# Kernel optimization log

Hardware: AMD Instinct MI355X
Metric: run time of the kernel (lower is better)

## Reference

```python
import jax, jax.numpy as jnp
import numpy as np

D_MODEL = 1024
NUM_HEADS = 16
HEAD_DIM = D_MODEL // NUM_HEADS  # used only for score scaling, as in the torch code


def setup_inputs() -> dict:
    key = jax.random.key(0)
    ks = jax.random.split(key, 8)
    B, S, D = 4, 2048, D_MODEL
    w_scale = 1.0 / np.sqrt(D)
    return {
        "x": jax.random.normal(ks[0], (B, S, D), dtype=jnp.float32),
        "Wq": jax.random.normal(ks[1], (D, D), dtype=jnp.float32) * w_scale,
        "bq": jnp.zeros((D,), dtype=jnp.float32),
        "Wk": jax.random.normal(ks[2], (D, D), dtype=jnp.float32) * w_scale,
        "bk": jnp.zeros((D,), dtype=jnp.float32),
        "Wv": jax.random.normal(ks[3], (D, D), dtype=jnp.float32) * w_scale,
        "bv": jnp.zeros((D,), dtype=jnp.float32),
        "temperature_scale": jnp.ones((1,), dtype=jnp.float32),
    }


def reference(x, Wq, bq, Wk, bk, Wv, bv, temperature_scale):
    # q, k, v: (B, S, D) -- no head split in the original module
    q = x @ Wq + bq
    k = x @ Wk + bk
    v = x @ Wv + bv
    scale = jnp.asarray(HEAD_DIM, x.dtype) ** 0.5
    # scores: (B, S, S)
    scores = jnp.einsum("bqd,bkd->bqk", q, k) / scale / temperature_scale[0]
    probs = jax.nn.softmax(scores, axis=-1)
    # per-row attention entropy (B, S, 1)
    entropy = -jnp.sum(probs * jnp.log(probs + 1e-8), axis=-1, keepdims=True)
    attention_output = jnp.einsum("bqk,bkd->bqd", probs, v)
    return attention_output, entropy.mean()
```

## Files before the change

kernel.cpp:

```cpp
#include <hip/hip_runtime.h>
#include <hip/hip_bf16.h>
#include <cstdint>
#include <cstddef>


typedef __attribute__((ext_vector_type(8))) short short8;
typedef __attribute__((ext_vector_type(4))) short short4v;
typedef __attribute__((ext_vector_type(4))) float f32x4;

#define GLOBAL_AS __attribute__((address_space(1)))
#define LDS_AS __attribute__((address_space(3)))

__device__ __forceinline__ void async_load16(const void* g, void* lds) {
  __builtin_amdgcn_global_load_lds((GLOBAL_AS void*)g, (LDS_AS void*)lds, 16, 0, 0);
}

__device__ __forceinline__ short f2bf_s(float x) {
  __hip_bfloat16 h = __float2bfloat16(x);
  return *reinterpret_cast<short*>(&h);
}

template <int MODE>
__device__ __forceinline__
void gemm_body(const __hip_bfloat16* __restrict__ A,
               const __hip_bfloat16* __restrict__ Bt,
               void* __restrict__ Cout,
               const float* __restrict__ bias,
               int K, int lda, int ldb, int ldc,
               __hip_bfloat16* __restrict__ sA,
               __hip_bfloat16* __restrict__ sB,
               int m0, int n0,
               const float* __restrict__ aux,
               float* __restrict__ stats) {
  const int tid  = threadIdx.x;
  const int lane = tid & 63;
  const int wid  = tid >> 6;
  const int wm = (wid >> 1) * 64;
  const int wn = (wid & 1) * 64;
  const int quad = lane >> 4;
  const int rc   = lane & 15;

  f32x4 acc[4][4] = {};

  const int srow = tid >> 2;
  const int scol = ((tid & 3) ^ ((tid >> 3) & 3)) * 8;
  const __hip_bfloat16* Ag0 = A  + (size_t)(m0 + srow) * lda + scol;
  const __hip_bfloat16* Ag1 = Ag0 + (size_t)64 * lda;
  const __hip_bfloat16* Bg0 = Bt + (size_t)(n0 + srow) * ldb + scol;
  const __hip_bfloat16* Bg1 = Bg0 + (size_t)64 * ldb;
  __hip_bfloat16* sA0 = &sA[wid * 512];
  __hip_bfloat16* sA1 = &sA[2048 + wid * 512];
  __hip_bfloat16* sB0 = &sB[wid * 512];
  __hip_bfloat16* sB1 = &sB[2048 + wid * 512];

  const int q_sw = (quad ^ ((rc >> 1) & 3)) * 8;

  for (int k0 = 0; k0 < K; k0 += 32) {
    async_load16(Ag0 + k0, sA0);
    async_load16(Ag1 + k0, sA1);
    async_load16(Bg0 + k0, sB0);
    async_load16(Bg1 + k0, sB1);
    __syncthreads();

    short8 af[4], bf[4];
#pragma unroll
    for (int i = 0; i < 4; ++i)
      af[i] = *(const short8*)&sA[(wm + i * 16 + rc) * 32 + q_sw];
#pragma unroll
    for (int i = 0; i < 4; ++i)
      bf[i] = *(const short8*)&sB[(wn + i * 16 + rc) * 32 + q_sw];

#pragma unroll
    for (int mi = 0; mi < 4; ++mi)
#pragma unroll
      for (int ni = 0; ni < 4; ++ni)
        acc[mi][ni] = __builtin_amdgcn_mfma_f32_16x16x32_bf16(
            af[mi], bf[ni], acc[mi][ni], 0, 0, 0);
    __syncthreads();
  }

  if (MODE == 3) {
    const float inv_scale = 1.0f / (8.0f * aux[0]);
    float l_acc[4][4] = {}, w_acc[4][4] = {};
#pragma unroll
    for (int mi = 0; mi < 4; ++mi)
#pragma unroll
      for (int ni = 0; ni < 4; ++ni)
#pragma unroll
        for (int r = 0; r < 4; ++r) {
          const float xv = acc[mi][ni][r] * inv_scale;
          const float e = __expf(xv);
          acc[mi][ni][r] = e;
          l_acc[mi][r] += e;
          w_acc[mi][r] += e * xv;
        }
    const int chunk = (n0 + wn) >> 6;
#pragma unroll
    for (int mi = 0; mi < 4; ++mi)
#pragma unroll
      for (int r = 0; r < 4; ++r) {
        float l = l_acc[mi][r], w = w_acc[mi][r];
#pragma unroll
        for (int off = 1; off < 16; off <<= 1) {
          l += __shfl_xor(l, off);
          w += __shfl_xor(w, off);
        }
        if (rc == 0) {
          const int row = m0 + wm + mi * 16 + quad * 4 + r;
          *(float2*)&stats[((size_t)row * 32 + chunk) * 2] = make_float2(l, w);
        }
      }
#pragma unroll
    for (int mi = 0; mi < 4; ++mi)
#pragma unroll
      for (int ni = 0; ni < 4; ++ni) {
        const int col = n0 + wn + ni * 16 + rc;
#pragma unroll
        for (int r = 0; r < 4; ++r) {
          const int row = m0 + wm + mi * 16 + quad * 4 + r;
          ((__hip_bfloat16*)Cout)[(size_t)row * ldc + col] =
              __float2bfloat16(acc[mi][ni][r]);
        }
      }
  } else if (MODE == 4) {
#pragma unroll
    for (int mi = 0; mi < 4; ++mi) {
      float sc[4];
#pragma unroll
      for (int r = 0; r < 4; ++r)
        sc[r] = aux[m0 + wm + mi * 16 + quad * 4 + r];
#pragma unroll
      for (int ni = 0; ni < 4; ++ni) {
        const int col = n0 + wn + ni * 16 + rc;
#pragma unroll
        for (int r = 0; r < 4; ++r) {
          const int row = m0 + wm + mi * 16 + quad * 4 + r;
          ((float*)Cout)[(size_t)row * ldc + col] = acc[mi][ni][r] * sc[r];
        }
      }
    }
  } else {
#pragma unroll
    for (int mi = 0; mi < 4; ++mi) {
#pragma unroll
      for (int ni = 0; ni < 4; ++ni) {
        const int col = n0 + wn + ni * 16 + rc;
        const float badd = bias[col];
        if (MODE == 2) {
          const int rowb = m0 + wm + mi * 16 + quad * 4;
          short4v o;
#pragma unroll
          for (int r = 0; r < 4; ++r) o[r] = f2bf_s(acc[mi][ni][r] + badd);
          const size_t idx = (size_t)(rowb >> 11) * (1024u * 2048u) +
                             (size_t)col * 2048u + (size_t)(rowb & 2047);
          *(short4v*)((short*)Cout + idx) = o;
        } else {
#pragma unroll
          for (int r = 0; r < 4; ++r) {
            const int row = m0 + wm + mi * 16 + quad * 4 + r;
            ((__hip_bfloat16*)Cout)[(size_t)row * ldc + col] =
                __float2bfloat16(acc[mi][ni][r] + badd);
          }
        }
      }
    }
  }
}


__global__ __launch_bounds__(256)
void qkv_fused(const __hip_bfloat16* __restrict__ xb,
               const __hip_bfloat16* __restrict__ Wt,
               __hip_bfloat16* __restrict__ qb, __hip_bfloat16* __restrict__ kb,
               __hip_bfloat16* __restrict__ vt,
               const float* __restrict__ bq, const float* __restrict__ bk,
               const float* __restrict__ bv) {
  __shared__ __align__(16) __hip_bfloat16 sA[128 * 32];
  __shared__ __align__(16) __hip_bfloat16 sB[128 * 32];
  const int lin = blockIdx.x;
  const int j = lin & 7, t = lin >> 3;
  const int x = t & 7;
  const int G = j + 8 * (t >> 3);
  const int z = G >> 6, y = G & 63;
  const int m0 = y * 128, n0 = x * 128;

  const __hip_bfloat16* B = Wt + (size_t)z * 1024 * 1024;
  if (z == 0)
    gemm_body<1>(xb, B, qb, bq, 1024, 1024, 1024, 1024, sA, sB, m0, n0, nullptr, nullptr);
  else if (z == 1)
    gemm_body<1>(xb, B, kb, bk, 1024, 1024, 1024, 1024, sA, sB, m0, n0, nullptr, nullptr);
  else
    gemm_body<2>(xb, B, vt, bv, 1024, 1024, 1024, 0, sA, sB, m0, n0, nullptr, nullptr);
}

__global__ __launch_bounds__(256)
void scores_swz(const __hip_bfloat16* __restrict__ qb,
                const __hip_bfloat16* __restrict__ kb,
                __hip_bfloat16* __restrict__ Pt,
                const float* __restrict__ tptr,
                float* __restrict__ stats) {
  __shared__ __align__(16) __hip_bfloat16 sA[128 * 32];
  __shared__ __align__(16) __hip_bfloat16 sB[128 * 32];
  const int lin = blockIdx.x;
  const int j = lin & 7, t = lin >> 3;
  const int w = t & 15;
  const int G = j + 8 * (t >> 4);
  const size_t z = G >> 4;
  const int r = G & 15;
  const int y = (r >> 2) * 4 + (w >> 2);
  const int x = (r & 3) * 4 + (w & 3);
  gemm_body<3>(qb + z * 2048 * 1024, kb + z * 2048 * 1024,
               Pt + z * 2048 * 2048, nullptr, 1024, 1024, 1024, 2048,
               sA, sB, y * 128, x * 128, tptr, stats + z * 2048 * 64);
}

__global__ __launch_bounds__(256)
void pv_swz(const __hip_bfloat16* __restrict__ Pt,
            const __hip_bfloat16* __restrict__ vt,
            float* __restrict__ out,
            const float* __restrict__ inv_l) {
  __shared__ __align__(16) __hip_bfloat16 sA[128 * 32];
  __shared__ __align__(16) __hip_bfloat16 sB[128 * 32];
  const int lin = blockIdx.x;
  const int j = lin & 7, t = lin >> 3;
  const int w = t & 3;
  const int G = j + 8 * (t >> 2);
  const size_t z = G >> 5;
  const int r = G & 31;
  const int y = (r >> 2) * 2 + (w >> 1);
  const int x = (r & 3) * 2 + (w & 1);
  gemm_body<4>(Pt + z * 2048 * 2048, vt + z * 1024 * 2048,
               out + z * 2048 * 1024, nullptr, 2048, 2048, 2048, 1024,
               sA, sB, y * 128, x * 128, inv_l + z * 2048, nullptr);
}

__global__ __launch_bounds__(256)
void cast_f32_to_bf16(const float* __restrict__ src,
                      __hip_bfloat16* __restrict__ dst, int n) {
  const int i = (blockIdx.x * 256 + threadIdx.x) * 8;
  if (i >= n) return;
  const float4 a = *(const float4*)(src + i);
  const float4 b = *(const float4*)(src + i + 4);
  short8 o;
  o[0] = f2bf_s(a.x); o[1] = f2bf_s(a.y); o[2] = f2bf_s(a.z); o[3] = f2bf_s(a.w);
  o[4] = f2bf_s(b.x); o[5] = f2bf_s(b.y); o[6] = f2bf_s(b.z); o[7] = f2bf_s(b.w);
  *(short8*)((short*)dst + i) = o;
}

__global__ __launch_bounds__(256)
void transpose_cast_3w(const float* __restrict__ Wq, const float* __restrict__ Wk,
                       const float* __restrict__ Wv,
                       __hip_bfloat16* __restrict__ Wt) {
  __shared__ float tile[64][65];
  const int z = blockIdx.z;
  const float* src = (z == 0) ? Wq : (z == 1) ? Wk : Wv;
  __hip_bfloat16* dst = Wt + (size_t)z * 1024 * 1024;
  const int c0 = blockIdx.x * 64;
  const int r0 = blockIdx.y * 64;
  const int lane = threadIdx.x & 63;
  const int grp  = threadIdx.x >> 6;
#pragma unroll
  for (int i = 0; i < 16; ++i) {
    const int r = grp * 16 + i;
    tile[r][lane] = src[(size_t)(r0 + r) * 1024 + c0 + lane];
  }
  __syncthreads();
#pragma unroll
  for (int i = 0; i < 16; ++i) {
    const int r = grp * 16 + i;
    dst[(size_t)(c0 + r) * 1024 + r0 + lane] = __float2bfloat16(tile[lane][r]);
  }
}

__global__ __launch_bounds__(256)
void stats_reduce(const float* __restrict__ stats,
                  float* __restrict__ inv_l, float* __restrict__ Hrow) {
  const int row = blockIdx.x * 256 + threadIdx.x;
  const float* sp = stats + (size_t)row * 64;
  float l = 0.f, w = 0.f;
#pragma unroll
  for (int j = 0; j < 16; ++j) {
    const float4 a = *(const float4*)(sp + j * 4);
    l += a.x + a.z;
    w += a.y + a.w;
  }
  const float il = 1.0f / l;
  inv_l[row] = il;
  Hrow[row] = __logf(l) - w * il;
}

__global__ __launch_bounds__(256)
void reduce_entropy(const float* __restrict__ Hrow, float* __restrict__ out) {
  const int tid  = threadIdx.x;
  const int lane = tid & 63;
  const int wid  = tid >> 6;
  float s = 0.f;
#pragma unroll
  for (int j = 0; j < 8; ++j) {
    const float4 a = *(const float4*)(Hrow + j * 1024 + tid * 4);
    s += a.x + a.y + a.z + a.w;
  }
#pragma unroll
  for (int off = 1; off < 64; off <<= 1) s += __shfl_xor(s, off);
  __shared__ float red[4];
  if (lane == 0) red[wid] = s;
  __syncthreads();
  if (tid == 0)
    out[0] = (red[0] + red[1] + red[2] + red[3]) * (1.0f / 8192.0f);
}

extern "C" void kernel_launch(void* const* d_in, const int* in_sizes, int n_in,
                              void* d_out, int out_size, void* d_ws, size_t ws_size,
                              hipStream_t stream) {
  const float* x    = (const float*)d_in[0];
  const float* Wq   = (const float*)d_in[1];
  const float* bq   = (const float*)d_in[2];
  const float* Wk   = (const float*)d_in[3];
  const float* bk   = (const float*)d_in[4];
  const float* Wv   = (const float*)d_in[5];
  const float* bv   = (const float*)d_in[6];
  const float* temp = (const float*)d_in[7];
  float* out = (float*)d_out;
  char* ws = (char*)d_ws;

  __hip_bfloat16* qb    = (__hip_bfloat16*)(ws + 0);
  __hip_bfloat16* kb    = (__hip_bfloat16*)(ws + 16777216);
  __hip_bfloat16* vt    = (__hip_bfloat16*)(ws + 33554432);
  __hip_bfloat16* xb    = (__hip_bfloat16*)(ws + 50331648);
  __hip_bfloat16* Wt    = (__hip_bfloat16*)(ws + 67108864);
  __hip_bfloat16* Pt    = (__hip_bfloat16*)(ws + 73400320);
  float*          stats = (float*)(ws + 106954752);
  float*          inv_l = (float*)(ws + 109051904);
  float*          Hrow  = (float*)(ws + 109084672);

  cast_f32_to_bf16<<<4096, 256, 0, stream>>>(x, xb, 8388608);
  transpose_cast_3w<<<dim3(16, 16, 3), 256, 0, stream>>>(Wq, Wk, Wv, Wt);

  qkv_fused<<<1536, 256, 0, stream>>>(xb, Wt, qb, kb, vt, bq, bk, bv);

  scores_swz<<<1024, 256, 0, stream>>>(qb, kb, Pt, temp, stats);
  stats_reduce<<<32, 256, 0, stream>>>(stats, inv_l, Hrow);
  pv_swz<<<512, 256, 0, stream>>>(Pt, vt, out, inv_l);

  reduce_entropy<<<1, 256, 0, stream>>>(Hrow, out + 8388608);
}
```

Baseline: 274.6 us.

## Double K-tile depth to 64 and fold score scaling into Q projection

The shared GEMM body now stages a 64-wide K slice per iteration with an 8-way XOR swizzle, halving the number of barrier pairs per tile and issuing two MFMA rounds per sync. The 1/(sqrt(d)*temperature) score scale is applied once when Q is written instead of on every score element, and the scores epilogue is restructured per row-block to reduce live registers. LDS use doubles to 32 KB per block, which may lower occupancy, and rounding Q after scaling changes bf16 rounding slightly.

```diff
diff --git a/kernel.cpp b/kernel.cpp
--- a/kernel.cpp
+++ b/kernel.cpp
@@ -42,64 +42,58 @@
 
   f32x4 acc[4][4] = {};
 
-  const int srow = tid >> 2;
-  const int scol = ((tid & 3) ^ ((tid >> 3) & 3)) * 8;
-  const __hip_bfloat16* Ag0 = A  + (size_t)(m0 + srow) * lda + scol;
-  const __hip_bfloat16* Ag1 = Ag0 + (size_t)64 * lda;
-  const __hip_bfloat16* Bg0 = Bt + (size_t)(n0 + srow) * ldb + scol;
-  const __hip_bfloat16* Bg1 = Bg0 + (size_t)64 * ldb;
-  __hip_bfloat16* sA0 = &sA[wid * 512];
-  __hip_bfloat16* sA1 = &sA[2048 + wid * 512];
-  __hip_bfloat16* sB0 = &sB[wid * 512];
-  __hip_bfloat16* sB1 = &sB[2048 + wid * 512];
-
-  const int q_sw = (quad ^ ((rc >> 1) & 3)) * 8;
-
-  for (int k0 = 0; k0 < K; k0 += 32) {
-    async_load16(Ag0 + k0, sA0);
-    async_load16(Ag1 + k0, sA1);
-    async_load16(Bg0 + k0, sB0);
-    async_load16(Bg1 + k0, sB1);
+  const int srow = tid >> 3;
+  const int scol = ((tid & 7) ^ ((tid >> 3) & 7)) * 8;
+  const __hip_bfloat16* Ag = A  + (size_t)(m0 + srow) * lda + scol;
+  const __hip_bfloat16* Bg = Bt + (size_t)(n0 + srow) * ldb + scol;
+
+  for (int k0 = 0; k0 < K; k0 += 64) {
+#pragma unroll
+    for (int p = 0; p < 4; ++p) {
+      async_load16(Ag + k0 + (size_t)(32 * p) * lda, &sA[(wid * 64 + 256 * p) * 8]);
+      async_load16(Bg + k0 + (size_t)(32 * p) * ldb, &sB[(wid * 64 + 256 * p) * 8]);
+    }
     __syncthreads();
 
-    short8 af[4], bf[4];
-#pragma unroll
-    for (int i = 0; i < 4; ++i)
-      af[i] = *(const short8*)&sA[(wm + i * 16 + rc) * 32 + q_sw];
-#pragma unroll
-    for (int i = 0; i < 4; ++i)
-      bf[i] = *(const short8*)&sB[(wn + i * 16 + rc) * 32 + q_sw];
-
-#pragma unroll
-    for (int mi = 0; mi < 4; ++mi)
+#pragma unroll
+    for (int kk = 0; kk < 2; ++kk) {
+      const int xo = ((kk * 4 + quad) ^ (rc & 7)) * 8;
+      short8 af[4], bf[4];
+#pragma unroll
+      for (int i = 0; i < 4; ++i)
+        af[i] = *(const short8*)&sA[(wm + i * 16 + rc) * 64 + xo];
+#pragma unroll
+      for (int i = 0; i < 4; ++i)
+        bf[i] = *(const short8*)&sB[(wn + i * 16 + rc) * 64 + xo];
+
+#pragma unroll
+      for (int mi = 0; mi < 4; ++mi)
+#pragma unroll
+        for (int ni = 0; ni < 4; ++ni)
+          acc[mi][ni] = __builtin_amdgcn_mfma_f32_16x16x32_bf16(
+              af[mi], bf[ni], acc[mi][ni], 0, 0, 0);
+    }
+    __syncthreads();
+  }
+
+  if (MODE == 3) {
+    const int chunk = (n0 + wn) >> 6;
+#pragma unroll
+    for (int mi = 0; mi < 4; ++mi) {
+      float l_acc[4] = {}, w_acc[4] = {};
 #pragma unroll
       for (int ni = 0; ni < 4; ++ni)
-        acc[mi][ni] = __builtin_amdgcn_mfma_f32_16x16x32_bf16(
-            af[mi], bf[ni], acc[mi][ni], 0, 0, 0);
-    __syncthreads();
-  }
-
-  if (MODE == 3) {
-    const float inv_scale = 1.0f / (8.0f * aux[0]);
-    float l_acc[4][4] = {}, w_acc[4][4] = {};
-#pragma unroll
-    for (int mi = 0; mi < 4; ++mi)
-#pragma unroll
-      for (int ni = 0; ni < 4; ++ni)
 #pragma unroll
         for (int r = 0; r < 4; ++r) {
-          const float xv = acc[mi][ni][r] * inv_scale;
+          const float xv = acc[mi][ni][r];
           const float e = __expf(xv);
           acc[mi][ni][r] = e;
-          l_acc[mi][r] += e;
-          w_acc[mi][r] += e * xv;
-        }
-    const int chunk = (n0 + wn) >> 6;
-#pragma unroll
-    for (int mi = 0; mi < 4; ++mi)
+          l_acc[r] += e;
+          w_acc[r] += e * xv;
+        }
 #pragma unroll
       for (int r = 0; r < 4; ++r) {
-        float l = l_acc[mi][r], w = w_acc[mi][r];
+        float l = l_acc[r], w = w_acc[r];
 #pragma unroll
         for (int off = 1; off < 16; off <<= 1) {
           l += __shfl_xor(l, off);
@@ -110,8 +104,6 @@
           *(float2*)&stats[((size_t)row * 32 + chunk) * 2] = make_float2(l, w);
         }
       }
-#pragma unroll
-    for (int mi = 0; mi < 4; ++mi)
 #pragma unroll
       for (int ni = 0; ni < 4; ++ni) {
         const int col = n0 + wn + ni * 16 + rc;
@@ -122,6 +114,7 @@
               __float2bfloat16(acc[mi][ni][r]);
         }
       }
+    }
   } else if (MODE == 4) {
 #pragma unroll
     for (int mi = 0; mi < 4; ++mi) {
@@ -140,6 +133,7 @@
       }
     }
   } else {
+    const float qsc = (MODE == 1 && aux) ? 1.0f / (8.0f * aux[0]) : 1.0f;
 #pragma unroll
     for (int mi = 0; mi < 4; ++mi) {
 #pragma unroll
@@ -159,7 +153,7 @@
           for (int r = 0; r < 4; ++r) {
             const int row = m0 + wm + mi * 16 + quad * 4 + r;
             ((__hip_bfloat16*)Cout)[(size_t)row * ldc + col] =
-                __float2bfloat16(acc[mi][ni][r] + badd);
+                __float2bfloat16((acc[mi][ni][r] + badd) * qsc);
           }
         }
       }
@@ -174,9 +168,9 @@
                __hip_bfloat16* __restrict__ qb, __hip_bfloat16* __restrict__ kb,
                __hip_bfloat16* __restrict__ vt,
                const float* __restrict__ bq, const float* __restrict__ bk,
-               const float* __restrict__ bv) {
-  __shared__ __align__(16) __hip_bfloat16 sA[128 * 32];
-  __shared__ __align__(16) __hip_bfloat16 sB[128 * 32];
+               const float* __restrict__ bv, const float* __restrict__ tptr) {
+  __shared__ __align__(16) __hip_bfloat16 sA[128 * 64];
+  __shared__ __align__(16) __hip_bfloat16 sB[128 * 64];
   const int lin = blockIdx.x;
   const int j = lin & 7, t = lin >> 3;
   const int x = t & 7;
@@ -186,7 +180,7 @@
 
   const __hip_bfloat16* B = Wt + (size_t)z * 1024 * 1024;
   if (z == 0)
-    gemm_body<1>(xb, B, qb, bq, 1024, 1024, 1024, 1024, sA, sB, m0, n0, nullptr, nullptr);
+    gemm_body<1>(xb, B, qb, bq, 1024, 1024, 1024, 1024, sA, sB, m0, n0, tptr, nullptr);
   else if (z == 1)
     gemm_body<1>(xb, B, kb, bk, 1024, 1024, 1024, 1024, sA, sB, m0, n0, nullptr, nullptr);
   else
@@ -197,10 +191,9 @@
 void scores_swz(const __hip_bfloat16* __restrict__ qb,
                 const __hip_bfloat16* __restrict__ kb,
                 __hip_bfloat16* __restrict__ Pt,
-                const float* __restrict__ tptr,
                 float* __restrict__ stats) {
-  __shared__ __align__(16) __hip_bfloat16 sA[128 * 32];
-  __shared__ __align__(16) __hip_bfloat16 sB[128 * 32];
+  __shared__ __align__(16) __hip_bfloat16 sA[128 * 64];
+  __shared__ __align__(16) __hip_bfloat16 sB[128 * 64];
   const int lin = blockIdx.x;
   const int j = lin & 7, t = lin >> 3;
   const int w = t & 15;
@@ -211,7 +204,7 @@
   const int x = (r & 3) * 4 + (w & 3);
   gemm_body<3>(qb + z * 2048 * 1024, kb + z * 2048 * 1024,
                Pt + z * 2048 * 2048, nullptr, 1024, 1024, 1024, 2048,
-               sA, sB, y * 128, x * 128, tptr, stats + z * 2048 * 64);
+               sA, sB, y * 128, x * 128, nullptr, stats + z * 2048 * 64);
 }
 
 __global__ __launch_bounds__(256)
@@ -219,8 +212,8 @@
             const __hip_bfloat16* __restrict__ vt,
             float* __restrict__ out,
             const float* __restrict__ inv_l) {
-  __shared__ __align__(16) __hip_bfloat16 sA[128 * 32];
-  __shared__ __align__(16) __hip_bfloat16 sB[128 * 32];
+  __shared__ __align__(16) __hip_bfloat16 sA[128 * 64];
+  __shared__ __align__(16) __hip_bfloat16 sB[128 * 64];
   const int lin = blockIdx.x;
   const int j = lin & 7, t = lin >> 3;
   const int w = t & 3;
@@ -336,9 +329,9 @@
   cast_f32_to_bf16<<<4096, 256, 0, stream>>>(x, xb, 8388608);
   transpose_cast_3w<<<dim3(16, 16, 3), 256, 0, stream>>>(Wq, Wk, Wv, Wt);
 
-  qkv_fused<<<1536, 256, 0, stream>>>(xb, Wt, qb, kb, vt, bq, bk, bv);
-
-  scores_swz<<<1024, 256, 0, stream>>>(qb, kb, Pt, temp, stats);
+  qkv_fused<<<1536, 256, 0, stream>>>(xb, Wt, qb, kb, vt, bq, bk, bv, temp);
+
+  scores_swz<<<1024, 256, 0, stream>>>(qb, kb, Pt, stats);
   stats_reduce<<<32, 256, 0, stream>>>(stats, inv_l, Hrow);
   pv_swz<<<512, 256, 0, stream>>>(Pt, vt, out, inv_l);
 
```

New measurement: 261.9 us. 4.6% less time.
